# Kernel optimization log

Hardware: AMD Instinct MI355X
Metric: run time of the kernel (lower is better)

Reference implementation:

```python
import jax, jax.numpy as jnp
import numpy as np

ALPHA = 0.1   # leaky integration rate
NOISE = 0.02  # noise std
B, T, I, H, O = 64, 512, 128, 1024, 64


def setup_inputs() -> dict:
    key = jax.random.key(0)
    k1, k2, k3, k4, k5 = jax.random.split(key, 5)
    x = jax.random.normal(k1, (B, T, I), dtype=jnp.float32)
    wi = jax.random.normal(k2, (I, H), dtype=jnp.float32) / np.sqrt(I).astype(np.float32)
    wrec = jax.random.normal(k3, (H, H), dtype=jnp.float32) / np.sqrt(H).astype(np.float32)
    wo = jax.random.normal(k4, (H, O), dtype=jnp.float32) / np.sqrt(H).astype(np.float32)
    noise = jax.random.normal(k5, (B, T, H), dtype=jnp.float32)  # pre-sampled standard normal
    return {"x": x, "noise": noise, "wi": wi, "wrec": wrec, "wo": wo}


def reference(x, noise, wi, wrec, wo):
    # x: [B,T,I], noise: [B,T,H]; leaky tanh RNN scanned over time.
    batch = x.shape[0]
    h0 = jnp.zeros((batch, wrec.shape[0]), dtype=x.dtype)
    xs = jnp.swapaxes(x, 0, 1)       # [T,B,I]
    ns = jnpp if False else jnp.swapaxes(noise, 0, 1)  # [T,B,H]

    def step(h, inp):
        xt, nt = inp
        h = (1.0 - ALPHA) * h + ALPHA * (xt @ wi + jnp.tanh(h) @ wrec + nt * NOISE)
        return h, jnp.tanh(h) @ wo   # per-step output [B,O]

    _, outs = jax.lax.scan(step, h0, (xs, ns))  # outs: [T,B,O]
    return jnp.swapaxes(outs, 0, 1)  # [B,T,O]
```

## Files before the change

### kernel.cpp

```cpp
#include <hip/hip_runtime.h>
#include <hip/hip_bf16.h>


#define T_ 512
#define I_ 128
#define H_ 1024
#define O_ 64
#define GRPS 4
#define BG 16
#define NWG 128
#define POLL_CAP (1<<17)

#define GBUF_BYTES (GRPS*2*BG*H_*2)
#define STEPFLAG_OFF GBUF_BYTES
#define WS_NEED (GBUF_BYTES + 1024)

#define WREC_HI_E 0
#define WREC_LO_E 32768
#define WI_HI_E   65536
#define WI_LO_E   69632
#define WO_HI_E   73728
#define WO_LO_E   75776
#define RED_B     155648
#define REDO_B    161792
#define LDS_BYTES 162176

typedef __bf16 bf16x8 __attribute__((ext_vector_type(8)));
typedef float f32x4 __attribute__((ext_vector_type(4)));
typedef unsigned u32x4 __attribute__((ext_vector_type(4)));
typedef unsigned short u16;

__device__ __forceinline__ float fast_tanh(float v){
  float cx = fminf(fmaxf(v, -14.f), 14.f);
  float e = __builtin_amdgcn_exp2f(cx * 2.8853900817779268f);
  return 1.f - 2.f * __builtin_amdgcn_rcpf(e + 1.f);
}

__device__ __forceinline__ void flag_issue(unsigned& v, const u16* p){
  asm volatile("global_load_ushort %0, %1, off sc0 sc1" : "=v"(v) : "v"(p));
}
__device__ __forceinline__ unsigned sflag_load(const u16* p){
  unsigned v;
  asm volatile("global_load_ushort %0, %1, off sc0 sc1\n\ts_waitcnt vmcnt(0)"
               : "=v"(v) : "v"(p) : "memory");
  return v;
}
__device__ __forceinline__ void sflag_store(u16* p, unsigned v){
  asm volatile("global_store_short %0, %1, off sc0 sc1" :: "v"(p), "v"(v) : "memory");
}
__device__ __forceinline__ void g_load_frag(u32x4& d, const u16* p){
  asm volatile("global_load_dwordx4 %0, %1, off sc0 sc1" : "=v"(d) : "v"(p) : "memory");
}
__device__ __forceinline__ void g_store_u16(u16* p, unsigned v){
  asm volatile("global_store_short %0, %1, off sc0 sc1" :: "v"(p), "v"(v) : "memory");
}
__device__ __forceinline__ void g_store_f32(float* p, float v){
  asm volatile("global_store_dword %0, %1, off" :: "v"(p), "v"(v) : "memory");
}
__device__ __forceinline__ void gl_f32x4(f32x4& d, const float* p){
  asm volatile("global_load_dwordx4 %0, %1, off" : "=v"(d) : "v"(p));
}
__device__ __forceinline__ void gl_f32(float& d, const float* p){
  asm volatile("global_load_dword %0, %1, off" : "=v"(d) : "v"(p));
}
__device__ __forceinline__ void barrier_lds(){
  asm volatile("s_waitcnt lgkmcnt(0)\n\ts_barrier" ::: "memory");
}

__device__ void load_slice(const float* __restrict__ Wg, int ld, int c0, int K,
                           __bf16* hi, __bf16* lo){
  for (int idx = threadIdx.x; idx < K*32; idx += 256){
    int k = idx >> 5, c = idx & 31;
    float v = Wg[(size_t)k*ld + c0 + c];
    __bf16 h = (__bf16)v;
    __bf16 l = (__bf16)(v - (float)h);
    int kt = k >> 5, kin = k & 31, lg = kin >> 3, j = kin & 7;
    int off = (((kt*2 + (c>>4))*64 + (lg*16 + (c&15))) << 3) + j;
    hi[off] = h; lo[off] = l;
  }
}

#define MFMA __builtin_amdgcn_mfma_f32_16x16x32_bf16
#define BC(u) __builtin_bit_cast(bf16x8, u)

#define PACKX(v0, v1, xh, xl)                                      \
  { _Pragma("unroll")                                              \
    for (int jj = 0; jj < 4; ++jj){                                \
      float aa = (v0)[jj], bb = (v1)[jj];                          \
      __bf16 ah = (__bf16)aa, bh2 = (__bf16)bb;                    \
      (xh)[jj] = ah; (xh)[jj+4] = bh2;                             \
      (xl)[jj] = (__bf16)(aa - (float)ah);                         \
      (xl)[jj+4] = (__bf16)(bb - (float)bh2); } }

#define SEEDS(OA, OB)                                                          \
  { f32x4 nxA = {0.f,0.f,0.f,0.f}, nxB = {0.f,0.f,0.f,0.f};                    \
    _Pragma("unroll")                                                          \
    for (int kt = 0; kt < 4; ++kt){                                            \
      f32x4 v0 = (kt==0)?xv0:(kt==1)?xv2:(kt==2)?xv4:xv6;                      \
      f32x4 v1 = (kt==0)?xv1:(kt==1)?xv3:(kt==2)?xv5:xv7;                      \
      bf16x8 xh, xl; PACKX(v0, v1, xh, xl);                                    \
      bf16x8 wih = *(const bf16x8*)(B + WI_HI_E + kt*1024 + w*512 + bf);       \
      bf16x8 wil = *(const bf16x8*)(B + WI_LO_E + kt*1024 + w*512 + bf);       \
      nxA = MFMA(xh, wih, nxA, 0,0,0);                                         \
      nxB = MFMA(xl, wih, nxB, 0,0,0);                                         \
      nxA = MFMA(xh, wil, nxA, 0,0,0);                                         \
    }                                                                          \
    OA = nxA; OB = nxB; }

extern "C" __global__ __launch_bounds__(256, 1)
void rnn_kernel(const float* __restrict__ x, const float* __restrict__ noise,
                const float* __restrict__ wi, const float* __restrict__ wrec,
                const float* __restrict__ wo, float* __restrict__ out,
                u16* __restrict__ gbuf, u16* __restrict__ sflags)
{
  extern __shared__ char smem[];
  __bf16* B = (__bf16*)smem;
  float* REDN = (float*)(smem + RED_B);
  float* REDO = (float*)(smem + REDO_B);

  const int grp  = blockIdx.x >> 5;
  const int role = blockIdx.x & 31;
  const int c0 = role * 32;

  load_slice(wrec, H_, c0, H_, B + WREC_HI_E, B + WREC_LO_E);
  load_slice(wi,   H_, c0, I_, B + WI_HI_E,  B + WI_LO_E);
  for (int idx = threadIdx.x; idx < 2*H_; idx += 256){
    int col = idx >> 10, k = idx & (H_-1);
    float v = wo[(size_t)k*O_ + role*2 + col];
    __bf16 hh = (__bf16)v;
    B[WO_HI_E + col*H_ + k] = hh;
    B[WO_LO_E + col*H_ + k] = (__bf16)(v - (float)hh);
  }
  __syncthreads();

  const int lane = threadIdx.x & 63;
  const int w    = threadIdx.x >> 6;
  const int lhalf = lane >> 4;
  const int l15   = lane & 15;
  const int bf = lane * 8;
  const int wo_off = (l15 & 1)*1024 + lhalf*8;

  u16* gg = gbuf + grp * (2*BG*H_);
  u16* gf = sflags + grp * 64;
  const u16* pollp = gf + lane;
  const u16* abase = gg + (size_t)l15*H_ + w*256 + lhalf*8;

  const float* xrow  = x + (size_t)(grp*BG + l15)*T_*I_ + lhalf*8;
  const float* nrow0 = noise + (size_t)(grp*BG + lhalf*4)*T_*H_ + c0 + (w&1)*16 + l15;
  float* orow = out + (size_t)(grp*BG + lhalf*4)*T_*O_ + role*2 + (l15 & 1);

  f32x4 h0 = {0.f,0.f,0.f,0.f};
  f32x4 xA = {0.f,0.f,0.f,0.f}, xB = {0.f,0.f,0.f,0.f};
  u32x4 a[8];
  f32x4 xv0,xv1,xv2,xv3,xv4,xv5,xv6,xv7;
  float nz[4] = {0.f,0.f,0.f,0.f};

  if (w < 2){
    gl_f32x4(xv0, xrow);      gl_f32x4(xv1, xrow+4);
    gl_f32x4(xv2, xrow+32);   gl_f32x4(xv3, xrow+36);
    gl_f32x4(xv4, xrow+64);   gl_f32x4(xv5, xrow+68);
    gl_f32x4(xv6, xrow+96);   gl_f32x4(xv7, xrow+100);
    gl_f32(nz[0], nrow0);
    gl_f32(nz[1], nrow0 + (size_t)T_*H_);
    gl_f32(nz[2], nrow0 + 2*(size_t)T_*H_);
    gl_f32(nz[3], nrow0 + 3*(size_t)T_*H_);
    asm volatile("s_waitcnt vmcnt(0)"
      : "+v"(xv0),"+v"(xv1),"+v"(xv2),"+v"(xv3),
        "+v"(xv4),"+v"(xv5),"+v"(xv6),"+v"(xv7),
        "+v"(nz[0]),"+v"(nz[1]),"+v"(nz[2]),"+v"(nz[3]) :: "memory");
    __builtin_amdgcn_sched_barrier(0);
    SEEDS(xA, xB);
  }
  #pragma unroll
  for (int kt = 0; kt < 8; ++kt) g_load_frag(a[kt], abase + kt*32);
  barrier_lds();

  for (int i = 0; i < T_; ++i){
    asm volatile("s_waitcnt vmcnt(0)"
      : "+v"(a[0]),"+v"(a[1]),"+v"(a[2]),"+v"(a[3]),
        "+v"(a[4]),"+v"(a[5]),"+v"(a[6]),"+v"(a[7]) :: "memory");
    __builtin_amdgcn_sched_barrier(0);

    f32x4 c0A={0.f,0.f,0.f,0.f}, c0B={0.f,0.f,0.f,0.f};
    f32x4 c1A={0.f,0.f,0.f,0.f}, c1B={0.f,0.f,0.f,0.f};
    f32x4 oA ={0.f,0.f,0.f,0.f}, oB ={0.f,0.f,0.f,0.f};
    if (w == 0){ c0A = xA; c0B = xB; }
    if (w == 1){ c1A = xA; c1B = xB; }
    const int kb = w*8;
    #pragma unroll
    for (int kt = 0; kt < 8; ++kt){
      const int kg = kb + kt;
      bf16x8 bh0 = *(const bf16x8*)(B + WREC_HI_E + kg*1024 + bf);
      bf16x8 bl0 = *(const bf16x8*)(B + WREC_LO_E + kg*1024 + bf);
      bf16x8 bh1 = *(const bf16x8*)(B + WREC_HI_E + kg*1024 + 512 + bf);
      bf16x8 bl1 = *(const bf16x8*)(B + WREC_LO_E + kg*1024 + 512 + bf);
      bf16x8 wh  = *(const bf16x8*)(B + WO_HI_E + wo_off + kg*32);
      bf16x8 wl  = *(const bf16x8*)(B + WO_LO_E + wo_off + kg*32);
      bf16x8 av = BC(a[kt]);
      c0A = MFMA(av, bh0, c0A, 0,0,0);  c0B = MFMA(av, bl0, c0B, 0,0,0);
      c1A = MFMA(av, bh1, c1A, 0,0,0);  c1B = MFMA(av, bl1, c1B, 0,0,0);
      oA  = MFMA(av, wh,  oA,  0,0,0);  oB  = MFMA(av, wl,  oB,  0,0,0);
    }
    f32x4 cn0 = c0A + c0B, cn1 = c1A + c1B, co = oA + oB;

    float nz2[4] = {0.f,0.f,0.f,0.f};
    const bool more = (i+1 < T_);
    if (w < 2 && more){
      const float* xp = xrow + (size_t)(i+1)*I_;
      gl_f32x4(xv0, xp);      gl_f32x4(xv1, xp+4);
      gl_f32x4(xv2, xp+32);   gl_f32x4(xv3, xp+36);
      gl_f32x4(xv4, xp+64);   gl_f32x4(xv5, xp+68);
      gl_f32x4(xv6, xp+96);   gl_f32x4(xv7, xp+100);
      const float* np = nrow0 + (size_t)(i+1)*H_;
      gl_f32(nz2[0], np);
      gl_f32(nz2[1], np + (size_t)T_*H_);
      gl_f32(nz2[2], np + 2*(size_t)T_*H_);
      gl_f32(nz2[3], np + 3*(size_t)T_*H_);
    }

    if (w == 0){ *(f32x4*)&REDN[((1*3+0)*64+lane)*4] = cn1;
                 if (l15 < 2) *(f32x4*)&REDO[(0*8 + lhalf*2 + l15)*4] = co; }
    if (w == 1){ *(f32x4*)&REDN[((0*3+0)*64+lane)*4] = cn0;
                 if (l15 < 2) *(f32x4*)&REDO[(1*8 + lhalf*2 + l15)*4] = co; }
    if (w == 2){ *(f32x4*)&REDN[((0*3+1)*64+lane)*4] = cn0;
                 *(f32x4*)&REDN[((1*3+1)*64+lane)*4] = cn1; }
    if (w == 3){ *(f32x4*)&REDN[((0*3+2)*64+lane)*4] = cn0;
                 *(f32x4*)&REDN[((1*3+2)*64+lane)*4] = cn1;
                 if (l15 < 2) *(f32x4*)&REDO[(2*8 + lhalf*2 + l15)*4] = co; }
    barrier_lds();

    const unsigned tgt = (unsigned)(i+1);
    if (w < 2){
      const int fb = w ? 3 : 0;
      f32x4 s = w ? cn1 : cn0;
      s += *(f32x4*)&REDN[((fb+0)*64+lane)*4];
      s += *(f32x4*)&REDN[((fb+1)*64+lane)*4];
      s += *(f32x4*)&REDN[((fb+2)*64+lane)*4];
      u16* gp = gg + (size_t)((i+1)&1)*(BG*H_);
      #pragma unroll
      for (int r = 0; r < 4; ++r){
        int row = lhalf*4 + r;
        float hv = 0.9f*h0[r] + 0.1f*s[r] + 0.002f*nz[r];
        h0[r] = hv;
        u16 gv = __builtin_bit_cast(u16, (__bf16)fast_tanh(hv));
        g_store_u16(gp + (size_t)row*H_ + c0 + w*16 + l15, (unsigned)gv);
      }
      if (more){
        asm volatile("s_waitcnt vmcnt(0)"
          : "+v"(xv0),"+v"(xv1),"+v"(xv2),"+v"(xv3),
            "+v"(xv4),"+v"(xv5),"+v"(xv6),"+v"(xv7),
            "+v"(nz2[0]),"+v"(nz2[1]),"+v"(nz2[2]),"+v"(nz2[3]) :: "memory");
      } else {
        asm volatile("s_waitcnt vmcnt(0)" ::: "memory");
      }
      __builtin_amdgcn_sched_barrier(0);
      if (lane == 0) sflag_store(gf + role*2 + w, tgt);
      unsigned pv; flag_issue(pv, pollp);
      if (more){ SEEDS(xA, xB); }
      nz[0]=nz2[0]; nz[1]=nz2[1]; nz[2]=nz2[2]; nz[3]=nz2[3];
      asm volatile("s_waitcnt vmcnt(0)" : "+v"(pv) :: "memory");
      __builtin_amdgcn_sched_barrier(0);
      if (!__all((int)(pv >= tgt))){
        int guard = 0;
        while (true){
          unsigned v = sflag_load(pollp);
          if (__all((int)(v >= tgt))) break;
          if (++guard > POLL_CAP) break;
        }
      }
      {
        const u16* ap = abase + (size_t)((i+1)&1)*(BG*H_);
        #pragma unroll
        for (int kt = 0; kt < 8; ++kt) g_load_frag(a[kt], ap + kt*32);
      }
    } else if (w == 2){
      f32x4 so = {0.f,0.f,0.f,0.f};
      bool do_out = false;
      if (i > 0){
        f32x4 s = co;
        s += *(f32x4*)&REDO[(0*8 + lhalf*2 + l15)*4];
        s += *(f32x4*)&REDO[(1*8 + lhalf*2 + l15)*4];
        s += *(f32x4*)&REDO[(2*8 + lhalf*2 + l15)*4];
        so = s; do_out = (l15 < 2);
      }
      unsigned pv; flag_issue(pv, pollp);
      asm volatile("s_waitcnt vmcnt(0)" : "+v"(pv) :: "memory");
      __builtin_amdgcn_sched_barrier(0);
      if (!__all((int)(pv >= tgt))){
        int guard = 0;
        while (true){
          unsigned v = sflag_load(pollp);
          if (__all((int)(v >= tgt))) break;
          if (++guard > POLL_CAP) break;
        }
      }
      {
        const u16* ap = abase + (size_t)((i+1)&1)*(BG*H_);
        #pragma unroll
        for (int kt = 0; kt < 8; ++kt) g_load_frag(a[kt], ap + kt*32);
      }
      if (do_out){
        #pragma unroll
        for (int r = 0; r < 4; ++r)
          g_store_f32(orow + (size_t)r*T_*O_ + (size_t)(i-1)*O_, so[r]);
      }
    } else {
      unsigned pv; flag_issue(pv, pollp);
      asm volatile("s_waitcnt vmcnt(0)" : "+v"(pv) :: "memory");
      __builtin_amdgcn_sched_barrier(0);
      if (!__all((int)(pv >= tgt))){
        int guard = 0;
        while (true){
          unsigned v = sflag_load(pollp);
          if (__all((int)(v >= tgt))) break;
          if (++guard > POLL_CAP) break;
        }
      }
      {
        const u16* ap = abase + (size_t)((i+1)&1)*(BG*H_);
        #pragma unroll
        for (int kt = 0; kt < 8; ++kt) g_load_frag(a[kt], ap + kt*32);
      }
    }

    barrier_lds();
  }

  asm volatile("s_waitcnt vmcnt(0)"
    : "+v"(a[0]),"+v"(a[1]),"+v"(a[2]),"+v"(a[3]),
      "+v"(a[4]),"+v"(a[5]),"+v"(a[6]),"+v"(a[7]) :: "memory");
  __builtin_amdgcn_sched_barrier(0);
  {
    f32x4 oA={0.f,0.f,0.f,0.f}, oB={0.f,0.f,0.f,0.f};
    const int kb = w*8;
    #pragma unroll
    for (int kt = 0; kt < 8; ++kt){
      const int kg = kb + kt;
      bf16x8 wh = *(const bf16x8*)(B + WO_HI_E + wo_off + kg*32);
      bf16x8 wl = *(const bf16x8*)(B + WO_LO_E + wo_off + kg*32);
      bf16x8 av = BC(a[kt]);
      oA = MFMA(av, wh, oA, 0,0,0);  oB = MFMA(av, wl, oB, 0,0,0);
    }
    f32x4 co = oA + oB;
    if (l15 < 2){
      if (w == 0) *(f32x4*)&REDO[(0*8 + lhalf*2 + l15)*4] = co;
      if (w == 1) *(f32x4*)&REDO[(1*8 + lhalf*2 + l15)*4] = co;
      if (w == 3) *(f32x4*)&REDO[(2*8 + lhalf*2 + l15)*4] = co;
    }
    barrier_lds();
    if (w == 2 && l15 < 2){
      f32x4 s = co;
      s += *(f32x4*)&REDO[(0*8 + lhalf*2 + l15)*4];
      s += *(f32x4*)&REDO[(1*8 + lhalf*2 + l15)*4];
      s += *(f32x4*)&REDO[(2*8 + lhalf*2 + l15)*4];
      #pragma unroll
      for (int r = 0; r < 4; ++r)
        g_store_f32(orow + (size_t)r*T_*O_ + (size_t)(T_-1)*O_, s[r]);
    }
  }
  asm volatile("s_waitcnt vmcnt(0)" ::: "memory");
}

extern "C" void kernel_launch(void* const* d_in, const int* in_sizes, int n_in,
                              void* d_out, int out_size, void* d_ws, size_t ws_size,
                              hipStream_t stream){
  const float* x     = (const float*)d_in[0];
  const float* noise = (const float*)d_in[1];
  const float* wi    = (const float*)d_in[2];
  const float* wrec  = (const float*)d_in[3];
  const float* wo    = (const float*)d_in[4];
  float* out = (float*)d_out;

  if (ws_size < (size_t)WS_NEED) return;
  u16* gbuf = (u16*)d_ws;
  u16* sflags = (u16*)((char*)d_ws + STEPFLAG_OFF);

  hipMemsetAsync(d_ws, 0, WS_NEED, stream);

  hipFuncSetAttribute((const void*)rnn_kernel,
                      hipFuncAttributeMaxDynamicSharedMemorySize, LDS_BYTES);

  void* args[] = {(void*)&x, (void*)&noise, (void*)&wi, (void*)&wrec, (void*)&wo,
                  (void*)&out, (void*)&gbuf, (void*)&sflags};
  hipLaunchCooperativeKernel((const void*)rnn_kernel, dim3(NWG), dim3(256),
                             args, LDS_BYTES, stream);
}
```

Before: 2.776 ms.

## Split batch into eight groups of eight, stage noise through LDS

Changes the partition from 4 groups of 16 batch rows to 8 groups of 8 across 256 workgroups, so each group's persistent ring of 32 workgroups handles fewer rows and more CUs are used. Noise loading moves to wave 3, which prefetches the next step's values into a double-buffered LDS area. The x prefetch is issued earlier in the step. The MFMA tiles stay 16 rows wide, so half the rows are duplicated or wasted work. With 256 co-resident workgroups there are more flag pollers, which may add synchronization traffic.

After: 3.085 ms. 1.11x slower.

```diff
diff --git a/kernel.cpp b/kernel.cpp
--- a/kernel.cpp
+++ b/kernel.cpp
@@ -6,12 +6,10 @@
 #define I_ 128
 #define H_ 1024
 #define O_ 64
-#define GRPS 4
-#define BG 16
-#define NWG 128
+#define NWG 256
 #define POLL_CAP (1<<17)
 
-#define GBUF_BYTES (GRPS*2*BG*H_*2)
+#define GBUF_BYTES (8*2*8*H_*2)
 #define STEPFLAG_OFF GBUF_BYTES
 #define WS_NEED (GBUF_BYTES + 1024)
 
@@ -21,9 +19,9 @@
 #define WI_LO_E   69632
 #define WO_HI_E   73728
 #define WO_LO_E   75776
-#define RED_B     155648
-#define REDO_B    161792
-#define LDS_BYTES 162176
+#define RED_OFF_B   155648
+#define NS0_OFF_B   160256
+#define LDS_BYTES   162304
 
 typedef __bf16 bf16x8 __attribute__((ext_vector_type(8)));
 typedef float f32x4 __attribute__((ext_vector_type(4)));
@@ -115,8 +113,7 @@
 {
   extern __shared__ char smem[];
   __bf16* B = (__bf16*)smem;
-  float* REDN = (float*)(smem + RED_B);
-  float* REDO = (float*)(smem + REDO_B);
+  float* RED = (float*)(smem + RED_OFF_B);
 
   const int grp  = blockIdx.x >> 5;
   const int role = blockIdx.x & 31;
@@ -140,46 +137,73 @@
   const int bf = lane * 8;
   const int wo_off = (l15 & 1)*1024 + lhalf*8;
 
-  u16* gg = gbuf + grp * (2*BG*H_);
-  u16* gf = sflags + grp * 64;
+  u16* gg = gbuf + grp*(2*8*H_);
+  u16* gf = sflags + grp*64;
   const u16* pollp = gf + lane;
-  const u16* abase = gg + (size_t)l15*H_ + w*256 + lhalf*8;
-
-  const float* xrow  = x + (size_t)(grp*BG + l15)*T_*I_ + lhalf*8;
-  const float* nrow0 = noise + (size_t)(grp*BG + lhalf*4)*T_*H_ + c0 + (w&1)*16 + l15;
-  float* orow = out + (size_t)(grp*BG + lhalf*4)*T_*O_ + role*2 + (l15 & 1);
+  const u16* ab = gg + (size_t)(lane & 7)*H_ + w*256 + lhalf*8;
+  const float* xb = x + (size_t)(grp*8)*T_*I_;
+  const float* nb = noise + (size_t)(grp*8)*T_*H_;
+  float* ob = out + (size_t)(grp*8)*T_*O_;
 
   f32x4 h0 = {0.f,0.f,0.f,0.f};
   f32x4 xA = {0.f,0.f,0.f,0.f}, xB = {0.f,0.f,0.f,0.f};
   u32x4 a[8];
   f32x4 xv0,xv1,xv2,xv3,xv4,xv5,xv6,xv7;
-  float nz[4] = {0.f,0.f,0.f,0.f};
+  float n0,n1,n2,n3;
 
   if (w < 2){
-    gl_f32x4(xv0, xrow);      gl_f32x4(xv1, xrow+4);
-    gl_f32x4(xv2, xrow+32);   gl_f32x4(xv3, xrow+36);
-    gl_f32x4(xv4, xrow+64);   gl_f32x4(xv5, xrow+68);
-    gl_f32x4(xv6, xrow+96);   gl_f32x4(xv7, xrow+100);
-    gl_f32(nz[0], nrow0);
-    gl_f32(nz[1], nrow0 + (size_t)T_*H_);
-    gl_f32(nz[2], nrow0 + 2*(size_t)T_*H_);
-    gl_f32(nz[3], nrow0 + 3*(size_t)T_*H_);
+    const float* xp = xb + (size_t)(l15 & 7)*T_*I_ + lhalf*8;
+    gl_f32x4(xv0, xp);      gl_f32x4(xv1, xp+4);
+    gl_f32x4(xv2, xp+32);   gl_f32x4(xv3, xp+36);
+    gl_f32x4(xv4, xp+64);   gl_f32x4(xv5, xp+68);
+    gl_f32x4(xv6, xp+96);   gl_f32x4(xv7, xp+100);
     asm volatile("s_waitcnt vmcnt(0)"
       : "+v"(xv0),"+v"(xv1),"+v"(xv2),"+v"(xv3),
-        "+v"(xv4),"+v"(xv5),"+v"(xv6),"+v"(xv7),
-        "+v"(nz[0]),"+v"(nz[1]),"+v"(nz[2]),"+v"(nz[3]) :: "memory");
+        "+v"(xv4),"+v"(xv5),"+v"(xv6),"+v"(xv7) :: "memory");
     __builtin_amdgcn_sched_barrier(0);
     SEEDS(xA, xB);
+  } else if (w == 3){
+    const int b0 = lane >> 5, cc = lane & 31;
+    gl_f32(n0, nb + (size_t)(b0+0)*T_*H_ + c0 + cc);
+    gl_f32(n1, nb + (size_t)(b0+2)*T_*H_ + c0 + cc);
+    gl_f32(n2, nb + (size_t)(b0+4)*T_*H_ + c0 + cc);
+    gl_f32(n3, nb + (size_t)(b0+6)*T_*H_ + c0 + cc);
+    asm volatile("s_waitcnt vmcnt(0)"
+      : "+v"(n0),"+v"(n1),"+v"(n2),"+v"(n3) :: "memory");
+    __builtin_amdgcn_sched_barrier(0);
+    float* NS0 = (float*)(smem + NS0_OFF_B);
+    NS0[(b0+0)*32 + cc] = n0;
+    NS0[(b0+2)*32 + cc] = n1;
+    NS0[(b0+4)*32 + cc] = n2;
+    NS0[(b0+6)*32 + cc] = n3;
   }
   #pragma unroll
-  for (int kt = 0; kt < 8; ++kt) g_load_frag(a[kt], abase + kt*32);
+  for (int kt = 0; kt < 8; ++kt) g_load_frag(a[kt], ab + kt*32);
   barrier_lds();
 
   for (int i = 0; i < T_; ++i){
+    const bool more = (i+1 < T_);
+
     asm volatile("s_waitcnt vmcnt(0)"
       : "+v"(a[0]),"+v"(a[1]),"+v"(a[2]),"+v"(a[3]),
         "+v"(a[4]),"+v"(a[5]),"+v"(a[6]),"+v"(a[7]) :: "memory");
     __builtin_amdgcn_sched_barrier(0);
+
+    if (more){
+      if (w < 2){
+        const float* xp = xb + ((size_t)(l15 & 7)*T_ + (size_t)(i+1))*I_ + lhalf*8;
+        gl_f32x4(xv0, xp);      gl_f32x4(xv1, xp+4);
+        gl_f32x4(xv2, xp+32);   gl_f32x4(xv3, xp+36);
+        gl_f32x4(xv4, xp+64);   gl_f32x4(xv5, xp+68);
+        gl_f32x4(xv6, xp+96);   gl_f32x4(xv7, xp+100);
+      } else if (w == 3){
+        const int b0 = lane >> 5, cc = lane & 31;
+        gl_f32(n0, nb + ((size_t)(b0+0)*T_ + (i+1))*H_ + c0 + cc);
+        gl_f32(n1, nb + ((size_t)(b0+2)*T_ + (i+1))*H_ + c0 + cc);
+        gl_f32(n2, nb + ((size_t)(b0+4)*T_ + (i+1))*H_ + c0 + cc);
+        gl_f32(n3, nb + ((size_t)(b0+6)*T_ + (i+1))*H_ + c0 + cc);
+      }
+    }
 
     f32x4 c0A={0.f,0.f,0.f,0.f}, c0B={0.f,0.f,0.f,0.f};
     f32x4 c1A={0.f,0.f,0.f,0.f}, c1B={0.f,0.f,0.f,0.f};
@@ -203,63 +227,62 @@
     }
     f32x4 cn0 = c0A + c0B, cn1 = c1A + c1B, co = oA + oB;
 
-    float nz2[4] = {0.f,0.f,0.f,0.f};
-    const bool more = (i+1 < T_);
-    if (w < 2 && more){
-      const float* xp = xrow + (size_t)(i+1)*I_;
-      gl_f32x4(xv0, xp);      gl_f32x4(xv1, xp+4);
-      gl_f32x4(xv2, xp+32);   gl_f32x4(xv3, xp+36);
-      gl_f32x4(xv4, xp+64);   gl_f32x4(xv5, xp+68);
-      gl_f32x4(xv6, xp+96);   gl_f32x4(xv7, xp+100);
-      const float* np = nrow0 + (size_t)(i+1)*H_;
-      gl_f32(nz2[0], np);
-      gl_f32(nz2[1], np + (size_t)T_*H_);
-      gl_f32(nz2[2], np + 2*(size_t)T_*H_);
-      gl_f32(nz2[3], np + 3*(size_t)T_*H_);
-    }
-
-    if (w == 0){ *(f32x4*)&REDN[((1*3+0)*64+lane)*4] = cn1;
-                 if (l15 < 2) *(f32x4*)&REDO[(0*8 + lhalf*2 + l15)*4] = co; }
-    if (w == 1){ *(f32x4*)&REDN[((0*3+0)*64+lane)*4] = cn0;
-                 if (l15 < 2) *(f32x4*)&REDO[(1*8 + lhalf*2 + l15)*4] = co; }
-    if (w == 2){ *(f32x4*)&REDN[((0*3+1)*64+lane)*4] = cn0;
-                 *(f32x4*)&REDN[((1*3+1)*64+lane)*4] = cn1; }
-    if (w == 3){ *(f32x4*)&REDN[((0*3+2)*64+lane)*4] = cn0;
-                 *(f32x4*)&REDN[((1*3+2)*64+lane)*4] = cn1;
-                 if (l15 < 2) *(f32x4*)&REDO[(2*8 + lhalf*2 + l15)*4] = co; }
+    if (lane < 32){
+      if (w == 0){ *(f32x4*)&RED[((1*3+0)*32+lane)*4] = cn1; *(f32x4*)&RED[((2*3+0)*32+lane)*4] = co; }
+      if (w == 1){ *(f32x4*)&RED[((0*3+0)*32+lane)*4] = cn0; *(f32x4*)&RED[((2*3+1)*32+lane)*4] = co; }
+      if (w == 2){ *(f32x4*)&RED[((0*3+1)*32+lane)*4] = cn0; *(f32x4*)&RED[((1*3+1)*32+lane)*4] = cn1; }
+      if (w == 3){ *(f32x4*)&RED[((0*3+2)*32+lane)*4] = cn0; *(f32x4*)&RED[((1*3+2)*32+lane)*4] = cn1; *(f32x4*)&RED[((2*3+2)*32+lane)*4] = co; }
+    }
     barrier_lds();
 
-    const unsigned tgt = (unsigned)(i+1);
-    if (w < 2){
-      const int fb = w ? 3 : 0;
+    f32x4 so_out = {0.f,0.f,0.f,0.f};
+    bool do_out = false;
+    if (w < 2 && lane < 32){
+      const int fbase = w ? 3 : 0;
       f32x4 s = w ? cn1 : cn0;
-      s += *(f32x4*)&REDN[((fb+0)*64+lane)*4];
-      s += *(f32x4*)&REDN[((fb+1)*64+lane)*4];
-      s += *(f32x4*)&REDN[((fb+2)*64+lane)*4];
-      u16* gp = gg + (size_t)((i+1)&1)*(BG*H_);
+      s += *(f32x4*)&RED[((fbase+0)*32+lane)*4];
+      s += *(f32x4*)&RED[((fbase+1)*32+lane)*4];
+      s += *(f32x4*)&RED[((fbase+2)*32+lane)*4];
+      const float* NSr = (const float*)(smem + NS0_OFF_B + ((i & 1) << 10));
+      u16* gp = gg + (size_t)((i+1)&1)*(8*H_);
       #pragma unroll
       for (int r = 0; r < 4; ++r){
         int row = lhalf*4 + r;
-        float hv = 0.9f*h0[r] + 0.1f*s[r] + 0.002f*nz[r];
+        float hv = 0.9f*h0[r] + 0.1f*s[r] + 0.002f*NSr[row*32 + w*16 + l15];
         h0[r] = hv;
         u16 gv = __builtin_bit_cast(u16, (__bf16)fast_tanh(hv));
         g_store_u16(gp + (size_t)row*H_ + c0 + w*16 + l15, (unsigned)gv);
       }
-      if (more){
-        asm volatile("s_waitcnt vmcnt(0)"
-          : "+v"(xv0),"+v"(xv1),"+v"(xv2),"+v"(xv3),
-            "+v"(xv4),"+v"(xv5),"+v"(xv6),"+v"(xv7),
-            "+v"(nz2[0]),"+v"(nz2[1]),"+v"(nz2[2]),"+v"(nz2[3]) :: "memory");
-      } else {
-        asm volatile("s_waitcnt vmcnt(0)" ::: "memory");
-      }
-      __builtin_amdgcn_sched_barrier(0);
-      if (lane == 0) sflag_store(gf + role*2 + w, tgt);
-      unsigned pv; flag_issue(pv, pollp);
-      if (more){ SEEDS(xA, xB); }
-      nz[0]=nz2[0]; nz[1]=nz2[1]; nz[2]=nz2[2]; nz[3]=nz2[3];
-      asm volatile("s_waitcnt vmcnt(0)" : "+v"(pv) :: "memory");
-      __builtin_amdgcn_sched_barrier(0);
+    }
+    if (w == 2 && lane < 32 && i > 0){
+      f32x4 s = co;
+      s += *(f32x4*)&RED[((2*3+0)*32+lane)*4];
+      s += *(f32x4*)&RED[((2*3+1)*32+lane)*4];
+      s += *(f32x4*)&RED[((2*3+2)*32+lane)*4];
+      so_out = s;
+      do_out = (l15 < 2);
+    }
+
+    if (more && w < 2){
+      asm volatile("s_waitcnt vmcnt(0)"
+        : "+v"(xv0),"+v"(xv1),"+v"(xv2),"+v"(xv3),
+          "+v"(xv4),"+v"(xv5),"+v"(xv6),"+v"(xv7) :: "memory");
+    } else if (more && w == 3){
+      asm volatile("s_waitcnt vmcnt(0)"
+        : "+v"(n0),"+v"(n1),"+v"(n2),"+v"(n3) :: "memory");
+    } else {
+      asm volatile("s_waitcnt vmcnt(0)" ::: "memory");
+    }
+    __builtin_amdgcn_sched_barrier(0);
+
+    if (w < 2 && lane == 0) sflag_store(gf + role*2 + w, (unsigned)(i+1));
+
+    unsigned pv; flag_issue(pv, pollp);
+    if (w < 2 && more){ SEEDS(xA, xB); }
+    asm volatile("s_waitcnt vmcnt(0)" : "+v"(pv) :: "memory");
+    __builtin_amdgcn_sched_barrier(0);
+    {
+      const unsigned tgt = (unsigned)(i+1);
       if (!__all((int)(pv >= tgt))){
         int guard = 0;
         while (true){
@@ -268,59 +291,28 @@
           if (++guard > POLL_CAP) break;
         }
       }
-      {
-        const u16* ap = abase + (size_t)((i+1)&1)*(BG*H_);
-        #pragma unroll
-        for (int kt = 0; kt < 8; ++kt) g_load_frag(a[kt], ap + kt*32);
-      }
-    } else if (w == 2){
-      f32x4 so = {0.f,0.f,0.f,0.f};
-      bool do_out = false;
-      if (i > 0){
-        f32x4 s = co;
-        s += *(f32x4*)&REDO[(0*8 + lhalf*2 + l15)*4];
-        s += *(f32x4*)&REDO[(1*8 + lhalf*2 + l15)*4];
-        s += *(f32x4*)&REDO[(2*8 + lhalf*2 + l15)*4];
-        so = s; do_out = (l15 < 2);
-      }
-      unsigned pv; flag_issue(pv, pollp);
-      asm volatile("s_waitcnt vmcnt(0)" : "+v"(pv) :: "memory");
-      __builtin_amdgcn_sched_barrier(0);
-      if (!__all((int)(pv >= tgt))){
-        int guard = 0;
-        while (true){
-          unsigned v = sflag_load(pollp);
-          if (__all((int)(v >= tgt))) break;
-          if (++guard > POLL_CAP) break;
-        }
-      }
-      {
-        const u16* ap = abase + (size_t)((i+1)&1)*(BG*H_);
-        #pragma unroll
-        for (int kt = 0; kt < 8; ++kt) g_load_frag(a[kt], ap + kt*32);
-      }
+    }
+    {
+      const u16* ap = ab + (size_t)((i+1)&1)*(8*H_);
+      #pragma unroll
+      for (int kt = 0; kt < 8; ++kt) g_load_frag(a[kt], ap + kt*32);
+    }
+
+    if (w == 2){
       if (do_out){
         #pragma unroll
-        for (int r = 0; r < 4; ++r)
-          g_store_f32(orow + (size_t)r*T_*O_ + (size_t)(i-1)*O_, so[r]);
-      }
-    } else {
-      unsigned pv; flag_issue(pv, pollp);
-      asm volatile("s_waitcnt vmcnt(0)" : "+v"(pv) :: "memory");
-      __builtin_amdgcn_sched_barrier(0);
-      if (!__all((int)(pv >= tgt))){
-        int guard = 0;
-        while (true){
-          unsigned v = sflag_load(pollp);
-          if (__all((int)(v >= tgt))) break;
-          if (++guard > POLL_CAP) break;
+        for (int r = 0; r < 4; ++r){
+          int row = lhalf*4 + r;
+          g_store_f32(&ob[((size_t)row*T_ + (i-1))*O_ + role*2 + l15], so_out[r]);
         }
       }
-      {
-        const u16* ap = abase + (size_t)((i+1)&1)*(BG*H_);
-        #pragma unroll
-        for (int kt = 0; kt < 8; ++kt) g_load_frag(a[kt], ap + kt*32);
-      }
+    } else if (w == 3 && more){
+      float* NSw = (float*)(smem + NS0_OFF_B + (((i+1) & 1) << 10));
+      const int b0 = lane >> 5, cc = lane & 31;
+      NSw[(b0+0)*32 + cc] = n0;
+      NSw[(b0+2)*32 + cc] = n1;
+      NSw[(b0+4)*32 + cc] = n2;
+      NSw[(b0+6)*32 + cc] = n3;
     }
 
     barrier_lds();
@@ -342,20 +334,24 @@
       oA = MFMA(av, wh, oA, 0,0,0);  oB = MFMA(av, wl, oB, 0,0,0);
     }
     f32x4 co = oA + oB;
-    if (l15 < 2){
-      if (w == 0) *(f32x4*)&REDO[(0*8 + lhalf*2 + l15)*4] = co;
-      if (w == 1) *(f32x4*)&REDO[(1*8 + lhalf*2 + l15)*4] = co;
-      if (w == 3) *(f32x4*)&REDO[(2*8 + lhalf*2 + l15)*4] = co;
+    if (lane < 32){
+      if (w == 0) *(f32x4*)&RED[((2*3+0)*32+lane)*4] = co;
+      if (w == 1) *(f32x4*)&RED[((2*3+1)*32+lane)*4] = co;
+      if (w == 3) *(f32x4*)&RED[((2*3+2)*32+lane)*4] = co;
     }
     barrier_lds();
-    if (w == 2 && l15 < 2){
+    if (w == 2 && lane < 32){
       f32x4 s = co;
-      s += *(f32x4*)&REDO[(0*8 + lhalf*2 + l15)*4];
-      s += *(f32x4*)&REDO[(1*8 + lhalf*2 + l15)*4];
-      s += *(f32x4*)&REDO[(2*8 + lhalf*2 + l15)*4];
-      #pragma unroll
-      for (int r = 0; r < 4; ++r)
-        g_store_f32(orow + (size_t)r*T_*O_ + (size_t)(T_-1)*O_, s[r]);
+      s += *(f32x4*)&RED[((2*3+0)*32+lane)*4];
+      s += *(f32x4*)&RED[((2*3+1)*32+lane)*4];
+      s += *(f32x4*)&RED[((2*3+2)*32+lane)*4];
+      if (l15 < 2){
+        #pragma unroll
+        for (int r = 0; r < 4; ++r){
+          int row = lhalf*4 + r;
+          ob[((size_t)row*T_ + (T_-1))*O_ + role*2 + l15] = s[r];
+        }
+      }
     }
   }
   asm volatile("s_waitcnt vmcnt(0)" ::: "memory");
```
